# Kernel tuning notes

Measured on AMD Instinct MI355X. Metric: run time of the kernel, lower is better.

The kernel has to match this reference:

```python
import jax, jax.numpy as jnp
import numpy as np

LN_EPS = 1e-5
MIN_MASK_SUM = 1e-6


def setup_inputs() -> dict:
    key = jax.random.key(0)
    ks = jax.random.split(key, 8)
    B, N, D = 8, 576, 1024
    K, H, W = 64, 512, 512
    OUT, GEOM = 256, 5
    feature_map = jax.random.normal(ks[0], (B, N, D), dtype=jnp.float32)
    masks = jax.random.randint(ks[1], (B, K, H, W), 0, 2).astype(bool)
    s = 0.02
    w1 = jax.random.normal(ks[2], (D + GEOM, OUT), dtype=jnp.float32) * s
    b1 = jnp.zeros((OUT,), dtype=jnp.float32)
    ln_g = jnp.ones((OUT,), dtype=jnp.float32)
    ln_b = jnp.zeros((OUT,), dtype=jnp.float32)
    w2 = jax.random.normal(ks[3], (OUT, OUT), dtype=jnp.float32) * s
    b2 = jnp.zeros((OUT,), dtype=jnp.float32)
    return {"feature_map": feature_map, "masks": masks, "w1": w1, "b1": b1,
            "ln_g": ln_g, "ln_b": ln_b, "w2": w2, "b2": b2}


def _geom(masks):
    # masks: [B,K,H,W] bool -> [B,K,5] (cx, cy, area_norm, bbox_w, bbox_h)
    B, K, H, W = masks.shape
    mf = masks.astype(jnp.float32)
    area = mf.sum((-2, -1))                                  # [B,K]
    xg = jnp.arange(W, dtype=jnp.float32)
    yg = jnp.arange(H, dtype=jnp.float32)
    safe = jnp.maximum(area, 1.0)
    cx = jnp.einsum('bkhw,w->bk', mf, xg) / safe / W
    cy = jnp.einsum('bkhw,h->bk', mf, yg) / safe / H
    xs_any = masks.any(axis=2)                               # [B,K,W]
    ys_any = masks.any(axis=3)                               # [B,K,H]
    xi = jnp.arange(W, dtype=jnp.int32)
    yi = jnp.arange(H, dtype=jnp.int32)
    BIG = jnp.int32(1 << 30)
    xmin = jnp.min(jnp.where(xs_any, xi, BIG), -1)
    xmax = jnp.max(jnp.where(xs_any, xi, -1), -1)
    ymin = jnp.min(jnp.where(ys_any, yi, BIG), -1)
    ymax = jnp.max(jnp.where(ys_any, yi, -1), -1)
    bw = (xmax - xmin + 1).astype(jnp.float32) / W
    bh = (ymax - ymin + 1).astype(jnp.float32) / H
    geom = jnp.stack([cx, cy, area / (H * W), bw, bh], -1)   # [B,K,5]
    return jnp.where((area >= 1.0)[..., None], geom, 0.0)


def reference(feature_map, masks, w1, b1, ln_g, ln_b, w2, b2):
    B, N, D = feature_map.shape
    _, K, H, W = masks.shape
    Hf = int(round(N ** 0.5))
    # nearest-neighbor downsample of masks to the patch grid (torch 'nearest')
    ri = (jnp.arange(Hf) * H) // Hf
    ci = (jnp.arange(Hf) * W) // Hf
    m_small = masks[:, :, ri][:, :, :, ci].astype(jnp.float32).reshape(B, K, -1)  # [B,K,N]
    msum = jnp.maximum(m_small.sum(-1, keepdims=True), MIN_MASK_SUM)
    pooled = jnp.einsum('bkn,bnd->bkd', m_small, feature_map) / msum              # [B,K,D]
    pooled = pooled - feature_map.mean(axis=1, keepdims=True)                     # bg subtract
    geom = _geom(masks)                                                           # [B,K,5]
    x = jnp.concatenate([pooled, geom], axis=-1)                                  # [B,K,D+5]
    h = jax.nn.gelu(x @ w1 + b1, approximate=False)
    mu = h.mean(-1, keepdims=True)
    var = jnp.mean((h - mu) ** 2, axis=-1, keepdims=True)
    h = (h - mu) * jax.lax.rsqrt(var + LN_EPS) * ln_g + ln_b
    return h @ w2 + b2                                                            # [B,K,out]
```

## Files before the change

### kernel.cpp

```cpp
#include <hip/hip_runtime.h>
#include <math.h>

#define BB 8
#define NN 576
#define DD 1024
#define KK 64
#define HH 512
#define WW 512
#define OUTD 256
#define HF 24
#define XSTRIDE 1032

typedef int iv4 __attribute__((ext_vector_type(4)));

__global__ __launch_bounds__(1024) void k_geom(const int* __restrict__ masks,
                                               const float* __restrict__ fm,
                                               float* __restrict__ xbuf) {
    int bid = blockIdx.x;
    int b = bid & 7;
    int k = bid >> 3;
    int bk = b * KK + k;
    int tid = threadIdx.x;
    const int* mb = masks + (size_t)bk * (HH * WW);
    const iv4* mp = (const iv4*)mb;

    __shared__ __align__(16) float ms[NN];
    __shared__ float s_inv;
    __shared__ float rsum[16];
    __shared__ int r0[8], r1[8], r2[8], r3[8], r4[8], r5[8], r6[8];

    float msv = 0.f;
    if (tid < NN) {
        int i = tid / HF, j = tid - i * HF;
        int ri = (i * HH) / HF, ci = (j * WW) / HF;
        msv = (mb[ri * WW + ci] != 0) ? 1.f : 0.f;
        ms[tid] = msv;
    }
    {
        float v = msv;
        for (int off = 32; off > 0; off >>= 1) v += __shfl_down(v, off);
        if ((tid & 63) == 0) rsum[tid >> 6] = v;
    }
    __syncthreads();
    if (tid == 0) {
        float s = 0.f;
        for (int i = 0; i < 16; ++i) s += rsum[i];
        s_inv = 1.0f / fmaxf(s, 1e-6f);
    }
    __syncthreads();

    if (tid < 512) {
        const int stid = tid;
        const int y0 = stid >> 7;
        const int xb = (stid & 127) << 2;
        int cnt = 0, w3a = 0, syr = 0, colany = 0;
        int ymn_it = 1 << 20, ymx_it = -1;

        #pragma unroll 8
        for (int it = 0; it < 128; ++it) {
            iv4 m = __builtin_nontemporal_load(&mp[stid + (it << 9)]);
            int sum4 = m.x + m.y + m.z + m.w;
            int mask4 = m.x | (m.y << 1) | (m.z << 2) | (m.w << 3);
            cnt += sum4;
            w3a += m.y + (m.z << 1) + ((m.w << 1) + m.w);
            syr += sum4 * it;
            colany |= mask4;
            if (mask4) { ymn_it = min(ymn_it, it); ymx_it = it; }
        }

        int sx = xb * cnt + w3a;
        int sy = (syr << 2) + y0 * cnt;
        int xmn = colany ? xb + __builtin_ctz((unsigned)colany) : (1 << 30);
        int xmx = colany ? xb + (31 - __builtin_clz((unsigned)colany)) : -1;
        int ymn = (ymx_it >= 0) ? (ymn_it << 2) + y0 : (1 << 30);
        int ymx = (ymx_it >= 0) ? (ymx_it << 2) + y0 : -1;

        for (int off = 32; off > 0; off >>= 1) {
            cnt += __shfl_down(cnt, off);
            sx  += __shfl_down(sx,  off);
            sy  += __shfl_down(sy,  off);
            xmn = min(xmn, __shfl_down(xmn, off));
            xmx = max(xmx, __shfl_down(xmx, off));
            ymn = min(ymn, __shfl_down(ymn, off));
            ymx = max(ymx, __shfl_down(ymx, off));
        }
        int wv = stid >> 6;
        if ((stid & 63) == 0) {
            r0[wv] = cnt; r1[wv] = sx; r2[wv] = sy;
            r3[wv] = xmn; r4[wv] = xmx; r5[wv] = ymn; r6[wv] = ymx;
        }
    } else {
        const int ptid = tid - 512;
        const float* fp0 = fm + (size_t)b * NN * DD + ptid;
        const float* fp1 = fp0 + 512;
        float acc0 = 0.f, acc1 = 0.f, facc0 = 0.f, facc1 = 0.f;

        for (int c = 0; c < NN; c += 8) {
            float4 ma = *(const float4*)&ms[c];
            float4 mbq = *(const float4*)&ms[c + 4];
            float fa[8], fb[8];
            #pragma unroll
            for (int r = 0; r < 8; ++r) {
                fa[r] = fp0[(size_t)(c + r) * DD];
                fb[r] = fp1[(size_t)(c + r) * DD];
            }
            facc0 += fa[0] + fa[1] + fa[2] + fa[3] + fa[4] + fa[5] + fa[6] + fa[7];
            facc1 += fb[0] + fb[1] + fb[2] + fb[3] + fb[4] + fb[5] + fb[6] + fb[7];
            acc0 = fmaf(ma.x,  fa[0], acc0); acc0 = fmaf(ma.y,  fa[1], acc0);
            acc0 = fmaf(ma.z,  fa[2], acc0); acc0 = fmaf(ma.w,  fa[3], acc0);
            acc0 = fmaf(mbq.x, fa[4], acc0); acc0 = fmaf(mbq.y, fa[5], acc0);
            acc0 = fmaf(mbq.z, fa[6], acc0); acc0 = fmaf(mbq.w, fa[7], acc0);
            acc1 = fmaf(ma.x,  fb[0], acc1); acc1 = fmaf(ma.y,  fb[1], acc1);
            acc1 = fmaf(ma.z,  fb[2], acc1); acc1 = fmaf(ma.w,  fb[3], acc1);
            acc1 = fmaf(mbq.x, fb[4], acc1); acc1 = fmaf(mbq.y, fb[5], acc1);
            acc1 = fmaf(mbq.z, fb[6], acc1); acc1 = fmaf(mbq.w, fb[7], acc1);
        }

        float* xp = xbuf + (size_t)bk * XSTRIDE;
        xp[ptid]       = acc0 * s_inv - facc0 * (1.0f / 576.0f);
        xp[ptid + 512] = acc1 * s_inv - facc1 * (1.0f / 576.0f);
    }
    __syncthreads();

    if (tid == 0) {
        int cnt = r0[0], sx = r1[0], sy = r2[0];
        int xmn = r3[0], xmx = r4[0], ymn = r5[0], ymx = r6[0];
        for (int i = 1; i < 8; ++i) {
            cnt += r0[i]; sx += r1[i]; sy += r2[i];
            xmn = min(xmn, r3[i]); xmx = max(xmx, r4[i]);
            ymn = min(ymn, r5[i]); ymx = max(ymx, r6[i]);
        }
        float* gp = xbuf + (size_t)bk * XSTRIDE + DD;
        if (cnt >= 1) {
            float area = (float)cnt;
            gp[0] = (float)sx / area * (1.0f / 512.0f);
            gp[1] = (float)sy / area * (1.0f / 512.0f);
            gp[2] = area * (1.0f / 262144.0f);
            gp[3] = (float)(xmx - xmn + 1) * (1.0f / 512.0f);
            gp[4] = (float)(ymx - ymn + 1) * (1.0f / 512.0f);
        } else {
            gp[0] = 0.f; gp[1] = 0.f; gp[2] = 0.f; gp[3] = 0.f; gp[4] = 0.f;
        }
        gp[5] = 0.f; gp[6] = 0.f; gp[7] = 0.f;
    }
}

__global__ __launch_bounds__(512) void k_mlp(const float* __restrict__ xbuf,
                                             const float* __restrict__ w1,
                                             const float* __restrict__ b1,
                                             const float* __restrict__ ln_g,
                                             const float* __restrict__ ln_b,
                                             const float* __restrict__ w2,
                                             const float* __restrict__ b2,
                                             float* __restrict__ out) {
    int row0 = blockIdx.x * 4;
    int tid = threadIdx.x;
    int w = tid >> 6, lane = tid & 63;
    int c4 = lane * 4;
    int col = tid & 255, rhalf = tid >> 8;

    __shared__ float xs[4][XSTRIDE];
    __shared__ float hp[8][4][OUTD];
    __shared__ float hs[4][OUTD];

    for (int i = tid; i < 4 * (XSTRIDE / 4); i += 512) {
        int r = i / (XSTRIDE / 4), cq = i % (XSTRIDE / 4);
        *(float4*)&xs[r][cq * 4] =
            *(const float4*)&xbuf[(size_t)(row0 + r) * XSTRIDE + cq * 4];
    }
    __syncthreads();

    float acc[4][4] = {};
    int js = w * 128;
    int je = (w == 7) ? 1029 : js + 128;
    int j = js;
    for (; j + 4 <= je; j += 4) {
        float4 xv0 = *(const float4*)&xs[0][j];
        float4 xv1 = *(const float4*)&xs[1][j];
        float4 xv2 = *(const float4*)&xs[2][j];
        float4 xv3 = *(const float4*)&xs[3][j];
#define STEPA(jj, X0, X1, X2, X3)                                              \
        {                                                                      \
            float4 wv = *(const float4*)&w1[(size_t)(j + jj) * OUTD + c4];     \
            acc[0][0] += X0 * wv.x; acc[0][1] += X0 * wv.y;                    \
            acc[0][2] += X0 * wv.z; acc[0][3] += X0 * wv.w;                    \
            acc[1][0] += X1 * wv.x; acc[1][1] += X1 * wv.y;                    \
            acc[1][2] += X1 * wv.z; acc[1][3] += X1 * wv.w;                    \
            acc[2][0] += X2 * wv.x; acc[2][1] += X2 * wv.y;                    \
            acc[2][2] += X2 * wv.z; acc[2][3] += X2 * wv.w;                    \
            acc[3][0] += X3 * wv.x; acc[3][1] += X3 * wv.y;                    \
            acc[3][2] += X3 * wv.z; acc[3][3] += X3 * wv.w;                    \
        }
        STEPA(0, xv0.x, xv1.x, xv2.x, xv3.x)
        STEPA(1, xv0.y, xv1.y, xv2.y, xv3.y)
        STEPA(2, xv0.z, xv1.z, xv2.z, xv3.z)
        STEPA(3, xv0.w, xv1.w, xv2.w, xv3.w)
    }
    for (; j < je; ++j) {
        float xv[4] = {xs[0][j], xs[1][j], xs[2][j], xs[3][j]};
        #pragma unroll
        for (int ci = 0; ci < 4; ++ci) {
            float wvv = w1[(size_t)j * OUTD + c4 + ci];
            #pragma unroll
            for (int r = 0; r < 4; ++r) acc[r][ci] += xv[r] * wvv;
        }
    }
    #pragma unroll
    for (int r = 0; r < 4; ++r)
        *(float4*)&hp[w][r][c4] = make_float4(acc[r][0], acc[r][1], acc[r][2], acc[r][3]);
    __syncthreads();

    float h2[2];
    float b1v = b1[col];
    #pragma unroll
    for (int r2 = 0; r2 < 2; ++r2) {
        int r = rhalf * 2 + r2;
        float s = b1v;
        #pragma unroll
        for (int ww = 0; ww < 8; ++ww) s += hp[ww][r][col];
        h2[r2] = 0.5f * s * (1.0f + erff(s * 0.70710678118654752f));
    }
    __shared__ float s1[8][2], s2[8][2];
    #pragma unroll
    for (int r2 = 0; r2 < 2; ++r2) {
        float a = h2[r2], q = h2[r2] * h2[r2];
        for (int off = 32; off > 0; off >>= 1) {
            a += __shfl_down(a, off);
            q += __shfl_down(q, off);
        }
        if (lane == 0) { s1[w][r2] = a; s2[w][r2] = q; }
    }
    __syncthreads();
    __shared__ float mu_[4], rsd_[4];
    if (tid < 4) {
        int rh = tid >> 1, r2 = tid & 1;
        float a = 0.f, q = 0.f;
        #pragma unroll
        for (int i = 0; i < 4; ++i) {
            a += s1[rh * 4 + i][r2];
            q += s2[rh * 4 + i][r2];
        }
        float mu = a * (1.0f / 256.0f);
        float var = q * (1.0f / 256.0f) - mu * mu;
        mu_[tid] = mu;
        rsd_[tid] = rsqrtf(var + 1e-5f);
    }
    __syncthreads();
    float gv = ln_g[col], bv = ln_b[col];
    #pragma unroll
    for (int r2 = 0; r2 < 2; ++r2) {
        int r = rhalf * 2 + r2;
        hs[r][col] = (h2[r2] - mu_[r]) * rsd_[r] * gv + bv;
    }
    __syncthreads();

    float a2[4][4] = {};
    int j2 = w * 32;
    for (int g = 0; g < 8; ++g, j2 += 4) {
        float4 h0 = *(const float4*)&hs[0][j2];
        float4 h1 = *(const float4*)&hs[1][j2];
        float4 h2v = *(const float4*)&hs[2][j2];
        float4 h3 = *(const float4*)&hs[3][j2];
#define STEPB(jj, X0, X1, X2, X3)                                              \
        {                                                                      \
            float4 wv = *(const float4*)&w2[(size_t)(j2 + jj) * OUTD + c4];    \
            a2[0][0] += X0 * wv.x; a2[0][1] += X0 * wv.y;                      \
            a2[0][2] += X0 * wv.z; a2[0][3] += X0 * wv.w;                      \
            a2[1][0] += X1 * wv.x; a2[1][1] += X1 * wv.y;                      \
            a2[1][2] += X1 * wv.z; a2[1][3] += X1 * wv.w;                      \
            a2[2][0] += X2 * wv.x; a2[2][1] += X2 * wv.y;                      \
            a2[2][2] += X2 * wv.z; a2[2][3] += X2 * wv.w;                      \
            a2[3][0] += X3 * wv.x; a2[3][1] += X3 * wv.y;                      \
            a2[3][2] += X3 * wv.z; a2[3][3] += X3 * wv.w;                      \
        }
        STEPB(0, h0.x, h1.x, h2v.x, h3.x)
        STEPB(1, h0.y, h1.y, h2v.y, h3.y)
        STEPB(2, h0.z, h1.z, h2v.z, h3.z)
        STEPB(3, h0.w, h1.w, h2v.w, h3.w)
    }
    #pragma unroll
    for (int r = 0; r < 4; ++r)
        *(float4*)&hp[w][r][c4] = make_float4(a2[r][0], a2[r][1], a2[r][2], a2[r][3]);
    __syncthreads();

    float b2v = b2[col];
    #pragma unroll
    for (int r2 = 0; r2 < 2; ++r2) {
        int r = rhalf * 2 + r2;
        float o = b2v;
        #pragma unroll
        for (int ww = 0; ww < 8; ++ww) o += hp[ww][r][col];
        out[(size_t)(row0 + r) * OUTD + col] = o;
    }
}

extern "C" void kernel_launch(void* const* d_in, const int* in_sizes, int n_in,
                              void* d_out, int out_size, void* d_ws, size_t ws_size,
                              hipStream_t stream) {
    const float* fm    = (const float*)d_in[0];
    const int*   masks = (const int*)d_in[1];
    const float* w1    = (const float*)d_in[2];
    const float* b1    = (const float*)d_in[3];
    const float* ln_g  = (const float*)d_in[4];
    const float* ln_b  = (const float*)d_in[5];
    const float* w2    = (const float*)d_in[6];
    const float* b2    = (const float*)d_in[7];
    float* out = (float*)d_out;

    float* xbuf = (float*)d_ws;

    k_geom<<<512, 1024, 0, stream>>>(masks, fm, xbuf);
    k_mlp <<<128, 512, 0, stream>>>(xbuf, w1, b1, ln_g, ln_b, w2, b2, out);
}
```

Baseline: 143.2 us.

## Split mask-geometry and feature-pooling into separate 512-thread blocks by role

Measured after the change: 124.7 us. -12.9%, faster.

```diff
diff --git a/kernel.cpp b/kernel.cpp
--- a/kernel.cpp
+++ b/kernel.cpp
@@ -13,52 +13,33 @@
 
 typedef int iv4 __attribute__((ext_vector_type(4)));
 
-__global__ __launch_bounds__(1024) void k_geom(const int* __restrict__ masks,
-                                               const float* __restrict__ fm,
-                                               float* __restrict__ xbuf) {
-    int bid = blockIdx.x;
-    int b = bid & 7;
-    int k = bid >> 3;
-    int bk = b * KK + k;
-    int tid = threadIdx.x;
-    const int* mb = masks + (size_t)bk * (HH * WW);
-    const iv4* mp = (const iv4*)mb;
+__global__ __launch_bounds__(512, 4) void k_fused(const int* __restrict__ masks,
+                                                  const float* __restrict__ fm,
+                                                  float* __restrict__ xbuf) {
+    const int bid = blockIdx.x;
+    const int role = (bid >> 3) & 1;
+    const int s = bid & 7;
+    const int q = bid >> 4;
+    const int b = s, k = q;
+    const int bk = b * KK + k;
+    const int tid = threadIdx.x;
 
     __shared__ __align__(16) float ms[NN];
+    __shared__ float pacc[256][8];
+    __shared__ float rsum[8];
     __shared__ float s_inv;
-    __shared__ float rsum[16];
     __shared__ int r0[8], r1[8], r2[8], r3[8], r4[8], r5[8], r6[8];
 
-    float msv = 0.f;
-    if (tid < NN) {
-        int i = tid / HF, j = tid - i * HF;
-        int ri = (i * HH) / HF, ci = (j * WW) / HF;
-        msv = (mb[ri * WW + ci] != 0) ? 1.f : 0.f;
-        ms[tid] = msv;
-    }
-    {
-        float v = msv;
-        for (int off = 32; off > 0; off >>= 1) v += __shfl_down(v, off);
-        if ((tid & 63) == 0) rsum[tid >> 6] = v;
-    }
-    __syncthreads();
-    if (tid == 0) {
-        float s = 0.f;
-        for (int i = 0; i < 16; ++i) s += rsum[i];
-        s_inv = 1.0f / fmaxf(s, 1e-6f);
-    }
-    __syncthreads();
-
-    if (tid < 512) {
-        const int stid = tid;
-        const int y0 = stid >> 7;
-        const int xb = (stid & 127) << 2;
+    if (role == 0) {
+        const iv4* mp = (const iv4*)(masks + (size_t)bk * (HH * WW));
+        const int y0 = tid >> 7;
+        const int xb = (tid & 127) << 2;
         int cnt = 0, w3a = 0, syr = 0, colany = 0;
         int ymn_it = 1 << 20, ymx_it = -1;
 
         #pragma unroll 8
         for (int it = 0; it < 128; ++it) {
-            iv4 m = __builtin_nontemporal_load(&mp[stid + (it << 9)]);
+            iv4 m = __builtin_nontemporal_load(&mp[tid + (it << 9)]);
             int sum4 = m.x + m.y + m.z + m.w;
             int mask4 = m.x | (m.y << 1) | (m.z << 2) | (m.w << 3);
             cnt += sum4;
@@ -84,64 +65,96 @@
             ymn = min(ymn, __shfl_down(ymn, off));
             ymx = max(ymx, __shfl_down(ymx, off));
         }
-        int wv = stid >> 6;
-        if ((stid & 63) == 0) {
+        int wv = tid >> 6;
+        if ((tid & 63) == 0) {
             r0[wv] = cnt; r1[wv] = sx; r2[wv] = sy;
             r3[wv] = xmn; r4[wv] = xmx; r5[wv] = ymn; r6[wv] = ymx;
         }
+        __syncthreads();
+        if (tid == 0) {
+            for (int i = 1; i < 8; ++i) {
+                cnt += r0[i]; sx += r1[i]; sy += r2[i];
+                xmn = min(xmn, r3[i]); xmx = max(xmx, r4[i]);
+                ymn = min(ymn, r5[i]); ymx = max(ymx, r6[i]);
+            }
+            float* gp = xbuf + (size_t)bk * XSTRIDE + DD;
+            if (cnt >= 1) {
+                float area = (float)cnt;
+                gp[0] = (float)sx / area * (1.0f / 512.0f);
+                gp[1] = (float)sy / area * (1.0f / 512.0f);
+                gp[2] = area * (1.0f / 262144.0f);
+                gp[3] = (float)(xmx - xmn + 1) * (1.0f / 512.0f);
+                gp[4] = (float)(ymx - ymn + 1) * (1.0f / 512.0f);
+            } else {
+                gp[0] = 0.f; gp[1] = 0.f; gp[2] = 0.f; gp[3] = 0.f; gp[4] = 0.f;
+            }
+            gp[5] = 0.f; gp[6] = 0.f; gp[7] = 0.f;
+        }
     } else {
-        const int ptid = tid - 512;
-        const float* fp0 = fm + (size_t)b * NN * DD + ptid;
-        const float* fp1 = fp0 + 512;
-        float acc0 = 0.f, acc1 = 0.f, facc0 = 0.f, facc1 = 0.f;
-
-        for (int c = 0; c < NN; c += 8) {
-            float4 ma = *(const float4*)&ms[c];
-            float4 mbq = *(const float4*)&ms[c + 4];
-            float fa[8], fb[8];
-            #pragma unroll
-            for (int r = 0; r < 8; ++r) {
-                fa[r] = fp0[(size_t)(c + r) * DD];
-                fb[r] = fp1[(size_t)(c + r) * DD];
-            }
-            facc0 += fa[0] + fa[1] + fa[2] + fa[3] + fa[4] + fa[5] + fa[6] + fa[7];
-            facc1 += fb[0] + fb[1] + fb[2] + fb[3] + fb[4] + fb[5] + fb[6] + fb[7];
-            acc0 = fmaf(ma.x,  fa[0], acc0); acc0 = fmaf(ma.y,  fa[1], acc0);
-            acc0 = fmaf(ma.z,  fa[2], acc0); acc0 = fmaf(ma.w,  fa[3], acc0);
-            acc0 = fmaf(mbq.x, fa[4], acc0); acc0 = fmaf(mbq.y, fa[5], acc0);
-            acc0 = fmaf(mbq.z, fa[6], acc0); acc0 = fmaf(mbq.w, fa[7], acc0);
-            acc1 = fmaf(ma.x,  fb[0], acc1); acc1 = fmaf(ma.y,  fb[1], acc1);
-            acc1 = fmaf(ma.z,  fb[2], acc1); acc1 = fmaf(ma.w,  fb[3], acc1);
-            acc1 = fmaf(mbq.x, fb[4], acc1); acc1 = fmaf(mbq.y, fb[5], acc1);
-            acc1 = fmaf(mbq.z, fb[6], acc1); acc1 = fmaf(mbq.w, fb[7], acc1);
-        }
-
-        float* xp = xbuf + (size_t)bk * XSTRIDE;
-        xp[ptid]       = acc0 * s_inv - facc0 * (1.0f / 576.0f);
-        xp[ptid + 512] = acc1 * s_inv - facc1 * (1.0f / 576.0f);
-    }
-    __syncthreads();
-
-    if (tid == 0) {
-        int cnt = r0[0], sx = r1[0], sy = r2[0];
-        int xmn = r3[0], xmx = r4[0], ymn = r5[0], ymx = r6[0];
-        for (int i = 1; i < 8; ++i) {
-            cnt += r0[i]; sx += r1[i]; sy += r2[i];
-            xmn = min(xmn, r3[i]); xmx = max(xmx, r4[i]);
-            ymn = min(ymn, r5[i]); ymx = max(ymx, r6[i]);
-        }
-        float* gp = xbuf + (size_t)bk * XSTRIDE + DD;
-        if (cnt >= 1) {
-            float area = (float)cnt;
-            gp[0] = (float)sx / area * (1.0f / 512.0f);
-            gp[1] = (float)sy / area * (1.0f / 512.0f);
-            gp[2] = area * (1.0f / 262144.0f);
-            gp[3] = (float)(xmx - xmn + 1) * (1.0f / 512.0f);
-            gp[4] = (float)(ymx - ymn + 1) * (1.0f / 512.0f);
-        } else {
-            gp[0] = 0.f; gp[1] = 0.f; gp[2] = 0.f; gp[3] = 0.f; gp[4] = 0.f;
-        }
-        gp[5] = 0.f; gp[6] = 0.f; gp[7] = 0.f;
+        const int* mb = masks + (size_t)bk * (HH * WW);
+
+        float msv = 0.f;
+        {
+            int n = tid;
+            int i = n / HF, j = n - i * HF;
+            int ri = (i * HH) / HF, ci = (j * WW) / HF;
+            float v = (mb[ri * WW + ci] != 0) ? 1.f : 0.f;
+            ms[n] = v;
+            msv += v;
+        }
+        if (tid < NN - 512) {
+            int n = 512 + tid;
+            int i = n / HF, j = n - i * HF;
+            int ri = (i * HH) / HF, ci = (j * WW) / HF;
+            float v = (mb[ri * WW + ci] != 0) ? 1.f : 0.f;
+            ms[n] = v;
+            msv += v;
+        }
+        for (int off = 32; off > 0; off >>= 1) msv += __shfl_down(msv, off);
+        if ((tid & 63) == 0) rsum[tid >> 6] = msv;
+        __syncthreads();
+        if (tid == 0) {
+            float t = 0.f;
+            for (int i = 0; i < 8; ++i) t += rsum[i];
+            s_inv = 1.0f / fmaxf(t, 1e-6f);
+        }
+        __syncthreads();
+
+        const int c4i = tid & 255;
+        const int par = tid >> 8;
+        const float4* fp = (const float4*)(fm + (size_t)b * NN * DD) + c4i;
+        float4 acc = make_float4(0.f, 0.f, 0.f, 0.f);
+        float4 fac = make_float4(0.f, 0.f, 0.f, 0.f);
+        #pragma unroll 4
+        for (int n = par; n < NN; n += 2) {
+            float mn = ms[n];
+            float4 v = fp[(size_t)n * 256];
+            fac.x += v.x; fac.y += v.y; fac.z += v.z; fac.w += v.w;
+            acc.x = fmaf(mn, v.x, acc.x);
+            acc.y = fmaf(mn, v.y, acc.y);
+            acc.z = fmaf(mn, v.z, acc.z);
+            acc.w = fmaf(mn, v.w, acc.w);
+        }
+        if (par == 1) {
+            pacc[c4i][0] = acc.x; pacc[c4i][1] = acc.y;
+            pacc[c4i][2] = acc.z; pacc[c4i][3] = acc.w;
+            pacc[c4i][4] = fac.x; pacc[c4i][5] = fac.y;
+            pacc[c4i][6] = fac.z; pacc[c4i][7] = fac.w;
+        }
+        __syncthreads();
+        if (par == 0) {
+            acc.x += pacc[c4i][0]; acc.y += pacc[c4i][1];
+            acc.z += pacc[c4i][2]; acc.w += pacc[c4i][3];
+            fac.x += pacc[c4i][4]; fac.y += pacc[c4i][5];
+            fac.z += pacc[c4i][6]; fac.w += pacc[c4i][7];
+            float inv = s_inv;
+            float4 o;
+            o.x = acc.x * inv - fac.x * (1.0f / 576.0f);
+            o.y = acc.y * inv - fac.y * (1.0f / 576.0f);
+            o.z = acc.z * inv - fac.z * (1.0f / 576.0f);
+            o.w = acc.w * inv - fac.w * (1.0f / 576.0f);
+            *(float4*)&xbuf[(size_t)bk * XSTRIDE + 4 * c4i] = o;
+        }
     }
 }
 
@@ -215,33 +228,33 @@
     #pragma unroll
     for (int r2 = 0; r2 < 2; ++r2) {
         int r = rhalf * 2 + r2;
-        float s = b1v;
+        float sv = b1v;
         #pragma unroll
-        for (int ww = 0; ww < 8; ++ww) s += hp[ww][r][col];
-        h2[r2] = 0.5f * s * (1.0f + erff(s * 0.70710678118654752f));
+        for (int ww = 0; ww < 8; ++ww) sv += hp[ww][r][col];
+        h2[r2] = 0.5f * sv * (1.0f + erff(sv * 0.70710678118654752f));
     }
     __shared__ float s1[8][2], s2[8][2];
     #pragma unroll
     for (int r2 = 0; r2 < 2; ++r2) {
-        float a = h2[r2], q = h2[r2] * h2[r2];
+        float a = h2[r2], qv = h2[r2] * h2[r2];
         for (int off = 32; off > 0; off >>= 1) {
             a += __shfl_down(a, off);
-            q += __shfl_down(q, off);
-        }
-        if (lane == 0) { s1[w][r2] = a; s2[w][r2] = q; }
+            qv += __shfl_down(qv, off);
+        }
+        if (lane == 0) { s1[w][r2] = a; s2[w][r2] = qv; }
     }
     __syncthreads();
     __shared__ float mu_[4], rsd_[4];
     if (tid < 4) {
         int rh = tid >> 1, r2 = tid & 1;
-        float a = 0.f, q = 0.f;
+        float a = 0.f, qv = 0.f;
         #pragma unroll
         for (int i = 0; i < 4; ++i) {
             a += s1[rh * 4 + i][r2];
-            q += s2[rh * 4 + i][r2];
+            qv += s2[rh * 4 + i][r2];
         }
         float mu = a * (1.0f / 256.0f);
-        float var = q * (1.0f / 256.0f) - mu * mu;
+        float var = qv * (1.0f / 256.0f) - mu * mu;
         mu_[tid] = mu;
         rsd_[tid] = rsqrtf(var + 1e-5f);
     }
@@ -309,6 +322,6 @@
 
     float* xbuf = (float*)d_ws;
 
-    k_geom<<<512, 1024, 0, stream>>>(masks, fm, xbuf);
-    k_mlp <<<128, 512, 0, stream>>>(xbuf, w1, b1, ln_g, ln_b, w2, b2, out);
+    k_fused<<<1024, 512, 0, stream>>>(masks, fm, xbuf);
+    k_mlp  <<<128, 512, 0, stream>>>(xbuf, w1, b1, ln_g, ln_b, w2, b2, out);
 }
```
